# Performance work log

Measured on AMD Instinct MI355X. Metric: run time of the kernel, lower is better.

## Reference

```python
import jax, jax.numpy as jnp
import numpy as np

B, S, HID, NH, CACHE = 2, 1024, 1024, 16, 4096
HD = HID // NH
HOT = max(4, CACHE // 4)
COLD = CACHE - HOT
COMP = HID // 2
EPS = 1e-5


def setup_inputs() -> dict:
    key = jax.random.key(0)
    ks = jax.random.split(key, 16)
    std = 0.02
    inp = {
        'inputs': jax.random.normal(ks[0], (B, S, HID), jnp.float32),
        'hot_keys': std * jax.random.normal(ks[1], (HOT, HID), jnp.float32),
        'hot_values': std * jax.random.normal(ks[2], (HOT, HID), jnp.float32),
        'hot_age': jnp.zeros((HOT,), jnp.float32),
        'hot_access': jnp.zeros((HOT,), jnp.float32),
        'cold_keys': std * jax.random.normal(ks[3], (COLD, HID), jnp.float32),
        'cold_values': std * jax.random.normal(ks[4], (COLD, HID), jnp.float32),
        'cold_age': jnp.zeros((COLD,), jnp.float32),
        'cold_access': jnp.zeros((COLD,), jnp.float32),
        # linear weights stored [in, out] (y = x @ W + b)
        'Wq': std * jax.random.normal(ks[5], (HID, HID), jnp.float32),
        'bq': jnp.zeros((HID,), jnp.float32),
        'Wk': std * jax.random.normal(ks[6], (HID, HID), jnp.float32),
        'bk': jnp.zeros((HID,), jnp.float32),
        'Wv': std * jax.random.normal(ks[7], (HID, HID), jnp.float32),
        'bv': jnp.zeros((HID,), jnp.float32),
        'Wo': std * jax.random.normal(ks[8], (HID, HID), jnp.float32),
        'bo': jnp.zeros((HID,), jnp.float32),
        'Wc': (1.0 / np.sqrt(HID)) * jax.random.normal(ks[9], (HID, COMP), jnp.float32),
        'bc': jnp.zeros((COMP,), jnp.float32),
        'Wd': (1.0 / np.sqrt(COMP)) * jax.random.normal(ks[10], (COMP, HID), jnp.float32),
        'bd': jnp.zeros((HID,), jnp.float32),
        'gamma': jnp.ones((HID,), jnp.float32),
        'beta': jnp.zeros((HID,), jnp.float32),
    }
    return inp


def _cache_level(q, cache_k, v_flat, age, access, Wk, bk, Wo, bo):
    # q: [B, NH, S, HD]; cache_k/v_flat: [C, HID]
    C = cache_k.shape[0]
    k = (cache_k @ Wk + bk).reshape(C, NH, HD)
    v = v_flat.reshape(C, NH, HD)
    scores = jnp.einsum('bhsd,chd->bhsc', q, k) / np.sqrt(HD)
    scores = scores + (-0.1 * age + 0.05 * access)  # broadcast over [B,H,S,C]
    attn = jax.nn.softmax(scores, axis=-1)
    out = jnp.einsum('bhsc,chd->bhsd', attn, v)
    out = out.transpose(0, 2, 1, 3).reshape(q.shape[0], q.shape[2], HID)
    return out @ Wo + bo


def reference(inputs, hot_keys, hot_values, hot_age, hot_access,
              cold_keys, cold_values, cold_age, cold_access,
              Wq, bq, Wk, bk, Wv, bv, Wo, bo, Wc, bc, Wd, bd, gamma, beta):
    q = (inputs @ Wq + bq).reshape(B, S, NH, HD).transpose(0, 2, 1, 3)
    # hot tier: values through value_net
    hot_v = hot_values @ Wv + bv
    hot_out = _cache_level(q, hot_keys, hot_v, hot_age, hot_access, Wk, bk, Wo, bo)
    # cold tier: values through compressor -> decompressor
    cold_v = (cold_values @ Wc + bc) @ Wd + bd
    cold_out = _cache_level(q, cold_keys, cold_v, cold_age, cold_access, Wk, bk, Wo, bo)
    x = hot_out + cold_out
    mu = jnp.mean(x, axis=-1, keepdims=True)
    var = jnp.mean(jnp.square(x - mu), axis=-1, keepdims=True)
    return (x - mu) / jnp.sqrt(var + EPS) * gamma + beta
```

## Files before the change

### kernel.cpp

```cpp
#include <hip/hip_runtime.h>

#define BBATCH 2
#define SS   1024
#define HID  1024
#define NH   16
#define HD   64
#define HOT  1024
#define COLD 3072
#define COMP 512

typedef __attribute__((ext_vector_type(8))) short s8v;
typedef __attribute__((ext_vector_type(4))) float f4v;
typedef unsigned short u16;
typedef unsigned int   u32;

__device__ __forceinline__ float b2f(u16 u){ return __uint_as_float(((u32)u)<<16); }
__device__ __forceinline__ u16 f2b(float f){
  u32 u = __float_as_uint(f);
  u += 0x7FFF + ((u>>16)&1);
  return (u16)(u>>16);
}
__device__ __forceinline__ u32 pk2r(u32 a, u32 b){
  return __builtin_amdgcn_perm(b + 0x8000u, a + 0x8000u, 0x07060302u);
}
__device__ __forceinline__ float ldsc(const void* p, int i, int isf32){
  return isf32 ? ((const float*)p)[i] : b2f(((const u16*)p)[i]);
}

__global__ void detect_kernel(const u32* __restrict__ gamma_raw, u32* __restrict__ flag){
  if (threadIdx.x == 0) flag[0] = (gamma_raw[0] == 0x3F800000u) ? 1u : 0u;
}

__global__ __launch_bounds__(256) void bias_kernel(
    const void* __restrict__ h_age, const void* __restrict__ h_acc,
    const void* __restrict__ c_age, const void* __restrict__ c_acc,
    float* __restrict__ BiasH, float* __restrict__ BiasC, const u32* __restrict__ flag)
{
  const int f = (int)flag[0];
  const int i = blockIdx.x * 256 + threadIdx.x;
  if (i < HOT) BiasH[i] = -0.1f * ldsc(h_age, i, f) + 0.05f * ldsc(h_acc, i, f);
  const int j = i - HOT;
  if (j >= 0 && j < COLD) BiasC[j] = -0.1f * ldsc(c_age, j, f) + 0.05f * ldsc(c_acc, j, f);
}

struct CDesc { const void* S; u16* D; int tile0, pad; };
struct CBatch { CDesc d[5]; int nd; };

__global__ __launch_bounds__(256) void convert_multi(CBatch cb, const u32* __restrict__ flag)
{
  int di = 0;
  for (int i = 1; i < cb.nd; i++) if ((int)blockIdx.x >= cb.d[i].tile0) di = i;
  const CDesc g = cb.d[di];
  const int f = (int)flag[0];
  const size_t e0 = (size_t)(blockIdx.x - g.tile0) * 2048 + (size_t)threadIdx.x * 8;
  if (f) {
    const float* s = (const float*)g.S + e0;
    const uint4 x = *(const uint4*)s, y = *(const uint4*)(s + 4);
    *(uint4*)(g.D + e0) =
      (uint4){ pk2r(x.x,x.y), pk2r(x.z,x.w), pk2r(y.x,y.y), pk2r(y.z,y.w) };
  } else {
    *(uint4*)(g.D + e0) = *(const uint4*)((const u16*)g.S + e0);
  }
}

struct TDesc { const void* S; u16* D; int R, C, cshift, tile0; };
struct TBatch { TDesc d[6]; int nd; };

__global__ __launch_bounds__(256) void transpose_kernel(TBatch tb, const u32* __restrict__ flag)
{
  __shared__ __align__(16) u16 Tt[64][72];
  int di = 0;
  for (int i = 1; i < tb.nd; i++) if ((int)blockIdx.x >= tb.d[i].tile0) di = i;
  const TDesc g = tb.d[di];
  const int local = blockIdx.x - g.tile0;
  const int ty = local >> g.cshift;
  const int tx = local & ((1 << g.cshift) - 1);
  const int r0 = ty * 64, c0 = tx * 64;
  const int f = (int)flag[0];
  const int t = threadIdx.x;
  const int sr = t >> 2, sc = (t & 3) * 16;

  union { uint4 q[2]; u16 h[16]; } u;
  if (f) {
    const float* s = (const float*)g.S + (size_t)(r0 + sr) * g.C + c0 + sc;
    const uint4 a = *(const uint4*)s,     b = *(const uint4*)(s + 4);
    const uint4 c = *(const uint4*)(s + 8), d2 = *(const uint4*)(s + 12);
    u.q[0] = (uint4){ pk2r(a.x,a.y), pk2r(a.z,a.w), pk2r(b.x,b.y), pk2r(b.z,b.w) };
    u.q[1] = (uint4){ pk2r(c.x,c.y), pk2r(c.z,c.w), pk2r(d2.x,d2.y), pk2r(d2.z,d2.w) };
  } else {
    const u16* s = (const u16*)g.S + (size_t)(r0 + sr) * g.C + c0 + sc;
    u.q[0] = *(const uint4*)s;  u.q[1] = *(const uint4*)(s + 8);
  }
  #pragma unroll
  for (int i = 0; i < 16; i++) Tt[sc + i][sr] = u.h[i];
  __syncthreads();

  const int dc = t >> 2, dr = (t & 3) * 16;
  const uint4 o0 = *(const uint4*)&Tt[dc][dr];
  const uint4 o1 = *(const uint4*)&Tt[dc][dr + 8];
  u16* dp = g.D + (size_t)(c0 + dc) * g.R + r0 + dr;
  *(uint4*)dp = o0;  *(uint4*)(dp + 8) = o1;
}

#define BM 128
#define BN 64
#define BK 32
struct GemmDesc {
  const void* A; const u16* BT; const void* bias; u16* C;
  int aflag, bcol0, M, N, K, nxlog, tile0, ctrans;
  float bias_scale;
};
struct GemmBatch { GemmDesc d[6]; int nd; };

__global__ __launch_bounds__(256) void gemm_multi(GemmBatch bat, const u32* __restrict__ flag)
{
  __shared__ __align__(16) u16 As[BM][BK + 8];
  __shared__ __align__(16) u16 Bs[BN][BK + 8];

  int di = 0;
  for (int i = 1; i < bat.nd; i++) if ((int)blockIdx.x >= bat.d[i].tile0) di = i;
  const GemmDesc g = bat.d[di];
  const int local = blockIdx.x - g.tile0;
  const int ty = local >> g.nxlog;
  const int tx = local - (ty << g.nxlog);
  const int m0 = ty * BM, n0 = tx * BN;

  const int f  = (int)flag[0];
  const int af = g.aflag ? f : 0;

  const int tid  = threadIdx.x;
  const int lane = tid & 63, wave = tid >> 6;
  const int quad = lane >> 4, l15 = lane & 15;
  const int wy = wave >> 1, wx = wave & 1;

  f4v acc[4][2];
  #pragma unroll
  for (int i = 0; i < 4; i++)
    #pragma unroll
    for (int j = 0; j < 2; j++) acc[i][j] = (f4v){0.f,0.f,0.f,0.f};

  const int ar = tid >> 1, ac = (tid & 1) * 16;
  const int br = tid >> 2, bc = (tid & 3) * 8;

  uint4 a0, a1, a2, a3;
  uint4 b0;

  auto load_tile = [&](int kk) {
    if (af) {
      const float* s = (const float*)g.A + (size_t)(m0 + ar) * g.K + kk + ac;
      a0 = *(const uint4*)s;       a1 = *(const uint4*)(s + 4);
      a2 = *(const uint4*)(s + 8); a3 = *(const uint4*)(s + 12);
    } else {
      const u16* s = (const u16*)g.A + (size_t)(m0 + ar) * g.K + kk + ac;
      a0 = *(const uint4*)s;  a1 = *(const uint4*)(s + 8);
    }
    const u16* bs = g.BT + (size_t)(g.bcol0 + n0 + br) * g.K + kk + bc;
    b0 = *(const uint4*)bs;
  };

  load_tile(0);

  for (int k0 = 0; k0 < g.K; k0 += BK) {
    __syncthreads();
    if (af) {
      *(uint4*)&As[ar][ac] =
        (uint4){ pk2r(a0.x,a0.y), pk2r(a0.z,a0.w), pk2r(a1.x,a1.y), pk2r(a1.z,a1.w) };
      *(uint4*)&As[ar][ac + 8] =
        (uint4){ pk2r(a2.x,a2.y), pk2r(a2.z,a2.w), pk2r(a3.x,a3.y), pk2r(a3.z,a3.w) };
    } else {
      *(uint4*)&As[ar][ac] = a0;  *(uint4*)&As[ar][ac + 8] = a1;
    }
    *(uint4*)&Bs[br][bc] = b0;
    __syncthreads();

    if (k0 + BK < g.K) load_tile(k0 + BK);

    s8v afr[4], bfr[2];
    #pragma unroll
    for (int i = 0; i < 4; i++)
      afr[i] = *(const s8v*)&As[wy * 64 + i * 16 + l15][quad * 8];
    #pragma unroll
    for (int j = 0; j < 2; j++)
      bfr[j] = *(const s8v*)&Bs[wx * 32 + j * 16 + l15][quad * 8];

    #pragma unroll
    for (int j = 0; j < 2; j++)
      #pragma unroll
      for (int i = 0; i < 4; i++)
        acc[i][j] = __builtin_amdgcn_mfma_f32_16x16x32_bf16(afr[i], bfr[j], acc[i][j], 0, 0, 0);
  }

  if (g.ctrans) {
    #pragma unroll
    for (int j = 0; j < 2; j++) {
      const int col = n0 + wx * 32 + j * 16 + l15;
      const float bv = ldsc(g.bias, g.bcol0 + col, f) * g.bias_scale;
      #pragma unroll
      for (int i = 0; i < 4; i++) {
        const int row = m0 + wy * 64 + i * 16 + quad * 4;
        u16 t4[4];
        #pragma unroll
        for (int r = 0; r < 4; r++) t4[r] = f2b(acc[i][j][r] + bv);
        *(uint2*)&g.C[(size_t)col * g.M + row] = *(uint2*)t4;
      }
    }
  } else {
    #pragma unroll
    for (int j = 0; j < 2; j++) {
      const int col = n0 + wx * 32 + j * 16 + l15;
      const float bv = ldsc(g.bias, g.bcol0 + col, f) * g.bias_scale;
      #pragma unroll
      for (int i = 0; i < 4; i++) {
        const int row = m0 + wy * 64 + i * 16 + quad * 4;
        #pragma unroll
        for (int r = 0; r < 4; r++)
          g.C[(size_t)(row + r) * g.N + col] = f2b(acc[i][j][r] + bv);
      }
    }
  }
}

__global__ __launch_bounds__(256) void attn_kernel(
    const u16* __restrict__ Q,
    const u16* __restrict__ KHg, const u16* __restrict__ VHT,
    const u16* __restrict__ KCg, const u16* __restrict__ VCT,
    const float* __restrict__ BiasH, const float* __restrict__ BiasC,
    float* __restrict__ HotOut, float* __restrict__ ColdNum, float* __restrict__ ColdZ,
    int NG, int glog)
{
  __shared__ __align__(16) u16 Ks[64][72];
  __shared__ __align__(16) u16 Vs[64][72];
  __shared__ __align__(16) u16 Ps[64][72];

  const int tid  = threadIdx.x;
  const int lane = tid & 63, wave = tid >> 6;
  const int quad = lane >> 4, l15 = lane & 15;
  const int bx    = blockIdx.x;
  const int slice = bx & 3;
  const int sblk  = (bx >> 2) & 15;
  const int h     = (bx >> 6) & ((1 << glog) - 1);
  const int b     = bx >> (6 + glog);
  const int rowbase = b * SS + sblk * 64;
  const int hoff  = h * HD;
  const int myrow = wave * 16;

  const bool hot = (slice == 0);
  const u16*  Kt   = hot ? KHg : KCg;
  const u16*  Vt   = hot ? VHT : VCT;
  const float* Bias = hot ? BiasH : BiasC;
  const int   e0  = hot ? 0 : (slice - 1) * 1024;
  const int   ldv = hot ? HOT : COLD;

  const u16* qp = Q + (size_t)(rowbase + myrow + l15) * NG + hoff + quad * 8;
  const s8v aq0 = *(const s8v*)qp;
  const s8v aq1 = *(const s8v*)(qp + 32);

  const int rk = tid >> 2, sk = (tid & 3) * 16;
  const u16* kbase = Kt + (size_t)(e0 + rk) * NG + hoff + sk;
  const u16* vbase = Vt + (size_t)(hoff + rk) * ldv + e0 + sk;
  uint4 kr0 = *(const uint4*)kbase, kr1 = *(const uint4*)(kbase + 8);
  uint4 vr0 = *(const uint4*)vbase, vr1 = *(const uint4*)(vbase + 8);

  f4v o[4];
  #pragma unroll
  for (int j = 0; j < 4; j++) o[j] = (f4v){0.f,0.f,0.f,0.f};
  float z[4] = {0.f,0.f,0.f,0.f};

  for (int c0 = 0; c0 < 1024; c0 += 64) {
    __syncthreads();
    *(uint4*)&Ks[rk][sk] = kr0;  *(uint4*)&Ks[rk][sk + 8] = kr1;
    *(uint4*)&Vs[rk][sk] = vr0;  *(uint4*)&Vs[rk][sk + 8] = vr1;
    __syncthreads();
    if (c0 + 64 < 1024) {
      const u16* kn = kbase + (size_t)(c0 + 64) * NG;
      const u16* vn = vbase + (c0 + 64);
      kr0 = *(const uint4*)kn;  kr1 = *(const uint4*)(kn + 8);
      vr0 = *(const uint4*)vn;  vr1 = *(const uint4*)(vn + 8);
    }

    #pragma unroll
    for (int j = 0; j < 4; j++) {
      f4v s = (f4v){0.f,0.f,0.f,0.f};
      const s8v bk0 = *(const s8v*)&Ks[j * 16 + l15][quad * 8];
      const s8v bk1 = *(const s8v*)&Ks[j * 16 + l15][32 + quad * 8];
      s = __builtin_amdgcn_mfma_f32_16x16x32_bf16(aq0, bk0, s, 0, 0, 0);
      s = __builtin_amdgcn_mfma_f32_16x16x32_bf16(aq1, bk1, s, 0, 0, 0);
      const int cg = e0 + c0 + j * 16 + l15;
      const float bias = Bias[cg];
      #pragma unroll
      for (int r = 0; r < 4; r++) {
        const float ev = __expf(fminf(s[r] * 0.125f + bias, 30.f));
        z[r] += ev;
        Ps[myrow + quad * 4 + r][j * 16 + l15] =
            (u16)((__float_as_uint(ev) + 0x8000u) >> 16);
      }
    }
    const s8v ap0 = *(const s8v*)&Ps[myrow + l15][quad * 8];
    const s8v ap1 = *(const s8v*)&Ps[myrow + l15][32 + quad * 8];
    #pragma unroll
    for (int j = 0; j < 4; j++) {
      const s8v bv0 = *(const s8v*)&Vs[j * 16 + l15][quad * 8];
      const s8v bv1 = *(const s8v*)&Vs[j * 16 + l15][32 + quad * 8];
      o[j] = __builtin_amdgcn_mfma_f32_16x16x32_bf16(ap0, bv0, o[j], 0, 0, 0);
      o[j] = __builtin_amdgcn_mfma_f32_16x16x32_bf16(ap1, bv1, o[j], 0, 0, 0);
    }
  }

  #pragma unroll
  for (int m = 1; m < 16; m <<= 1)
    #pragma unroll
    for (int r = 0; r < 4; r++) z[r] += __shfl_xor(z[r], m, 64);

  if (hot) {
    float rz[4];
    #pragma unroll
    for (int r = 0; r < 4; r++) rz[r] = 1.0f / z[r];
    #pragma unroll
    for (int j = 0; j < 4; j++) {
      const int col = hoff + j * 16 + l15;
      #pragma unroll
      for (int r = 0; r < 4; r++) {
        const int row = rowbase + myrow + quad * 4 + r;
        HotOut[(size_t)row * NG + col] = o[j][r] * rz[r];
      }
    }
  } else {
    #pragma unroll
    for (int j = 0; j < 4; j++) {
      const int col = hoff + j * 16 + l15;
      #pragma unroll
      for (int r = 0; r < 4; r++) {
        const int row = rowbase + myrow + quad * 4 + r;
        atomicAdd(&ColdNum[(size_t)row * NG + col], o[j][r]);
      }
    }
    if (l15 == 0) {
      #pragma unroll
      for (int r = 0; r < 4; r++) {
        const int row = rowbase + myrow + quad * 4 + r;
        atomicAdd(&ColdZ[(size_t)row * (1 << glog) + h], z[r]);
      }
    }
  }
}

__global__ __launch_bounds__(256) void combine_kernel(
    const float* __restrict__ HotOut, float* __restrict__ ColdNum,
    float* __restrict__ ColdZ, u16* __restrict__ ATT,
    int att_ld, int att_c0, int NG, int glog)
{
  const int gid   = blockIdx.x * 256 + threadIdx.x;
  const int shift = 4 + glog;
  const int row   = gid >> shift;
  const int c4    = (gid & ((1 << shift) - 1)) << 2;
  const int h     = c4 >> 6;
  const int G     = 1 << glog;

  const float4 hv = *(const float4*)&HotOut[(size_t)row * NG + c4];
  float4* cp = (float4*)&ColdNum[(size_t)row * NG + c4];
  const float4 cn = *cp;
  const float zi = 1.0f / ColdZ[(size_t)row * G + h];

  u16 ov[4];
  ov[0] = f2b(hv.x + cn.x * zi); ov[1] = f2b(hv.y + cn.y * zi);
  ov[2] = f2b(hv.z + cn.z * zi); ov[3] = f2b(hv.w + cn.w * zi);
  *(uint2*)&ATT[(size_t)row * att_ld + att_c0 + c4] = *(uint2*)ov;

  *cp = (float4){0.f,0.f,0.f,0.f};
  if ((c4 & 63) == 0) ColdZ[(size_t)row * G + h] = 0.f;
}

__global__ __launch_bounds__(256) void ln_kernel(
    const u16* __restrict__ X, const void* __restrict__ gamma,
    const void* __restrict__ beta, void* __restrict__ outp,
    const u32* __restrict__ flag)
{
  __shared__ float red[4];
  const int f = (int)flag[0];
  const int row = blockIdx.x, tid = threadIdx.x;
  const u16* xr = X + (size_t)row * HID;

  float x[4];
  { union { uint2 q; u16 hx[4]; } bx2;
    bx2.q = *(const uint2*)(xr + tid * 4);
    #pragma unroll
    for (int i = 0; i < 4; i++) x[i] = b2f(bx2.hx[i]); }

  float s = x[0] + x[1] + x[2] + x[3];
  #pragma unroll
  for (int m = 1; m < 64; m <<= 1) s += __shfl_xor(s, m, 64);
  if ((tid & 63) == 0) red[tid >> 6] = s;
  __syncthreads();
  const float mu = (red[0] + red[1] + red[2] + red[3]) * (1.0f / HID);
  __syncthreads();

  float v = 0.f;
  #pragma unroll
  for (int i = 0; i < 4; i++) { const float d = x[i] - mu; v += d * d; }
  #pragma unroll
  for (int m = 1; m < 64; m <<= 1) v += __shfl_xor(v, m, 64);
  if ((tid & 63) == 0) red[tid >> 6] = v;
  __syncthreads();
  const float var  = (red[0] + red[1] + red[2] + red[3]) * (1.0f / HID);
  const float rstd = 1.0f / sqrtf(var + 1e-5f);

  #pragma unroll
  for (int i = 0; i < 4; i++) {
    const int col = tid * 4 + i;
    const float val = (x[i] - mu) * rstd * ldsc(gamma, col, f) + ldsc(beta, col, f);
    if (f) ((float*)outp)[(size_t)row * HID + col] = val;
    else   ((u16*) outp)[(size_t)row * HID + col] = f2b(val);
  }
}

extern "C" void kernel_launch(void* const* d_in, const int* in_sizes, int n_in,
                              void* d_out, int out_size, void* d_ws, size_t ws_size,
                              hipStream_t stream)
{
  const void* inputs      = d_in[0];
  const void* hot_keys    = d_in[1];
  const void* hot_values  = d_in[2];
  const void* hot_age     = d_in[3];
  const void* hot_access  = d_in[4];
  const void* cold_keys   = d_in[5];
  const void* cold_values = d_in[6];
  const void* cold_age    = d_in[7];
  const void* cold_access = d_in[8];
  const void* Wq = d_in[9];   const void* bq = d_in[10];
  const void* Wk = d_in[11];  const void* bk = d_in[12];
  const void* Wv = d_in[13];  const void* bv = d_in[14];
  const void* Wo = d_in[15];  const void* bo = d_in[16];
  const void* Wc = d_in[17];  const void* bc = d_in[18];
  const void* Wd = d_in[19];  const void* bd = d_in[20];
  const void* gamma = d_in[21];
  const void* beta  = d_in[22];

  const size_t FIX    = 256 + 16384;
  const size_t WT     = (size_t)10 * 1024 * 1024;
  const size_t COPIES = (size_t)10240 * 1024 * 2;
  const size_t XB     = (size_t)2048 * HID * 2;
  auto PART = [](int Gc){ return (size_t)2048 * (64 * Gc) * 8 + (size_t)2048 * Gc * 4; };
  auto BUFS = [](int Gc){ return (size_t)10240 * (64 * Gc) * 2; };
  auto MX   = [](size_t a, size_t b){ return a > b ? a : b; };

  int G = 0, docopy = 0;
  { const size_t needF = FIX + WT + MX(COPIES, MX(PART(16), XB)) + BUFS(16);
    if (ws_size >= needF) { G = 16; docopy = 1; } }
  for (int c = 8; c >= 2 && !G; c >>= 1)
    if (ws_size >= FIX + WT + COPIES + MX(PART(c), XB) + BUFS(c)) { G = c; docopy = 1; }
  for (int c = 8; c >= 2 && !G; c >>= 1)
    if (ws_size >= FIX + WT + MX(PART(c), XB) + BUFS(c)) { G = c; docopy = 0; }
  if (!G) return;
  const int glog = (G == 16) ? 4 : (G == 8 ? 3 : (G == 4 ? 2 : 1));
  const int NG = 64 * G;
  const bool full = (G == 16);

  char* base  = (char*)d_ws;
  u32*  flag  = (u32*)base;
  float* BiasH = (float*)(base + 256);
  float* BiasC = BiasH + HOT;
  u16* WqT = (u16*)(base + FIX);
  u16* WkT = WqT + (size_t)1024 * 1024;
  u16* WvT = WkT + (size_t)1024 * 1024;
  u16* WoT = WvT + (size_t)1024 * 1024;
  u16* WcT = WoT + (size_t)1024 * 1024;
  u16* WdT = WcT + (size_t)512 * 1024;
  char* rp0 = base + FIX + WT;

  u16* inputsB = (u16*)rp0;
  u16* hotkB   = inputsB + (size_t)2048 * 1024;
  u16* coldkB  = hotkB   + (size_t)1024 * 1024;
  u16* hotvB   = coldkB  + (size_t)3072 * 1024;
  u16* coldvB  = hotvB   + (size_t)1024 * 1024;

  char* rp = rp0 + ((docopy && !full) ? COPIES : 0);
  u16*   X       = (u16*)rp;
  float* HotOut  = (float*)rp;
  float* ColdNum = (float*)(rp + (size_t)2048 * NG * 4);
  float* ColdZ   = (float*)(rp + (size_t)2048 * NG * 8);
  const size_t Rbytes = full ? MX(COPIES, MX(PART(16), XB)) : MX(PART(G), XB);
  u16* Qg  = (u16*)(rp + Rbytes);
  u16* KHg = Qg  + (size_t)2048 * NG;
  u16* KCg = KHg + (size_t)HOT  * NG;
  u16* VHT = KCg + (size_t)COLD * NG;
  u16* VCT = VHT + (size_t)HOT  * NG;
  u16* ATT   = (u16*)d_out;
  u16* CVmid = (u16*)d_out + (size_t)2048 * 1024;

  const void* Aq = docopy ? (const void*)inputsB : inputs;
  const void* Ahk = docopy ? (const void*)hotkB  : hot_keys;
  const void* Ack = docopy ? (const void*)coldkB : cold_keys;
  const void* Ahv = docopy ? (const void*)hotvB  : hot_values;
  const void* Acv = docopy ? (const void*)coldvB : cold_values;
  const int afl = docopy ? 0 : 1;

  const dim3 blk(256);
  const int mQ = 2048 / BM, mH = HOT / BM, mC = COLD / BM;
  const size_t coldPart = (size_t)2048 * NG * 4 + (size_t)2048 * G * 4;

  detect_kernel<<<dim3(1), dim3(64), 0, stream>>>((const u32*)gamma, flag);
  bias_kernel<<<dim3((HOT + COLD) / 256), blk, 0, stream>>>(
      hot_age, hot_access, cold_age, cold_access, BiasH, BiasC, flag);

  if (docopy) {
    CBatch cb; cb.nd = 5; int t = 0;
    cb.d[0] = { inputs,      inputsB, t, 0 }; t += 1024;
    cb.d[1] = { hot_keys,    hotkB,   t, 0 }; t += 512;
    cb.d[2] = { cold_keys,   coldkB,  t, 0 }; t += 1536;
    cb.d[3] = { hot_values,  hotvB,   t, 0 }; t += 512;
    cb.d[4] = { cold_values, coldvB,  t, 0 }; t += 1536;
    convert_multi<<<dim3(t), blk, 0, stream>>>(cb, flag);
  }
  { TBatch tb; tb.nd = 6; int t = 0;
    tb.d[0] = { Wq, WqT, 1024, 1024, 4, t }; t += 256;
    tb.d[1] = { Wk, WkT, 1024, 1024, 4, t }; t += 256;
    tb.d[2] = { Wv, WvT, 1024, 1024, 4, t }; t += 256;
    tb.d[3] = { Wo, WoT, 1024, 1024, 4, t }; t += 256;
    tb.d[4] = { Wc, WcT, 1024,  512, 3, t }; t += 128;
    tb.d[5] = { Wd, WdT,  512, 1024, 4, t }; t += 128;
    transpose_kernel<<<dim3(t), blk, 0, stream>>>(tb, flag);
  }

  if (full) {
    { GemmBatch bb; bb.nd = 5; int t = 0;
      bb.d[0] = { Aq,  WqT, bq, Qg,    afl, 0, 2048, 1024, 1024, 4, t, 0, 1.0f }; t += 16 * mQ;
      bb.d[1] = { Ahk, WkT, bk, KHg,   afl, 0, HOT,  1024, 1024, 4, t, 0, 1.0f }; t += 16 * mH;
      bb.d[2] = { Ack, WkT, bk, KCg,   afl, 0, COLD, 1024, 1024, 4, t, 0, 1.0f }; t += 16 * mC;
      bb.d[3] = { Ahv, WvT, bv, VHT,   afl, 0, HOT,  1024, 1024, 4, t, 1, 1.0f }; t += 16 * mH;
      bb.d[4] = { Acv, WcT, bc, CVmid, afl, 0, COLD,  512, 1024, 3, t, 0, 1.0f }; t += 8 * mC;
      gemm_multi<<<dim3(t), blk, 0, stream>>>(bb, flag);
    }
    { GemmBatch bb; bb.nd = 1;
      bb.d[0] = { CVmid, WdT, bd, VCT, 0, 0, COLD, 1024, 512, 4, 0, 1, 1.0f };
      gemm_multi<<<dim3(16 * mC), blk, 0, stream>>>(bb, flag);
    }
    hipMemsetAsync(ColdNum, 0, coldPart, stream);
    attn_kernel<<<dim3(BBATCH * 16 * 16 * 4), blk, 0, stream>>>(
        Qg, KHg, VHT, KCg, VCT, BiasH, BiasC, HotOut, ColdNum, ColdZ, NG, glog);
    combine_kernel<<<dim3((2048 * (NG / 4)) / 256), blk, 0, stream>>>(
        HotOut, ColdNum, ColdZ, ATT, HID, 0, NG, glog);
  } else {
    hipMemsetAsync(ColdNum, 0, coldPart, stream);
    { GemmBatch bb; bb.nd = 5; int t = 0;
      bb.d[0] = { Aq,  WqT, bq, Qg,    afl, 0, 2048, NG,  1024, glog, t, 0, 1.0f }; t += G * mQ;
      bb.d[1] = { Ahk, WkT, bk, KHg,   afl, 0, HOT,  NG,  1024, glog, t, 0, 1.0f }; t += G * mH;
      bb.d[2] = { Ack, WkT, bk, KCg,   afl, 0, COLD, NG,  1024, glog, t, 0, 1.0f }; t += G * mC;
      bb.d[3] = { Ahv, WvT, bv, VHT,   afl, 0, HOT,  NG,  1024, glog, t, 1, 1.0f }; t += G * mH;
      bb.d[4] = { Acv, WcT, bc, CVmid, afl, 0, COLD, 512, 1024, 3,    t, 0, 1.0f }; t += 8 * mC;
      gemm_multi<<<dim3(t), blk, 0, stream>>>(bb, flag);
    }
    { GemmBatch bb; bb.nd = 1;
      bb.d[0] = { CVmid, WdT, bd, VCT, 0, 0, COLD, NG, 512, glog, 0, 1, 1.0f };
      gemm_multi<<<dim3(G * mC), blk, 0, stream>>>(bb, flag);
    }
    attn_kernel<<<dim3(BBATCH * G * 16 * 4), blk, 0, stream>>>(
        Qg, KHg, VHT, KCg, VCT, BiasH, BiasC, HotOut, ColdNum, ColdZ, NG, glog);
    combine_kernel<<<dim3((2048 * (NG / 4)) / 256), blk, 0, stream>>>(
        HotOut, ColdNum, ColdZ, ATT, HID, 0, NG, glog);

    for (int p = 1; p < NH / G; ++p) {
      const int c0 = p * NG;
      GemmBatch bb; bb.nd = 5; int t = 0;
      bb.d[0] = { Aq,    WqT, bq, Qg,  afl, c0, 2048, NG, 1024, glog, t, 0, 1.0f }; t += G * mQ;
      bb.d[1] = { Ahk,   WkT, bk, KHg, afl, c0, HOT,  NG, 1024, glog, t, 0, 1.0f }; t += G * mH;
      bb.d[2] = { Ack,   WkT, bk, KCg, afl, c0, COLD, NG, 1024, glog, t, 0, 1.0f }; t += G * mC;
      bb.d[3] = { Ahv,   WvT, bv, VHT, afl, c0, HOT,  NG, 1024, glog, t, 1, 1.0f }; t += G * mH;
      bb.d[4] = { CVmid, WdT, bd, VCT, 0,   c0, COLD, NG, 512,  glog, t, 1, 1.0f }; t += G * mC;
      gemm_multi<<<dim3(t), blk, 0, stream>>>(bb, flag);

      attn_kernel<<<dim3(BBATCH * G * 16 * 4), blk, 0, stream>>>(
          Qg, KHg, VHT, KCg, VCT, BiasH, BiasC, HotOut, ColdNum, ColdZ, NG, glog);
      combine_kernel<<<dim3((2048 * (NG / 4)) / 256), blk, 0, stream>>>(
          HotOut, ColdNum, ColdZ, ATT, HID, c0, NG, glog);
    }
  }

  { GemmBatch bb; bb.nd = 1;
    bb.d[0] = { ATT, WoT, bo, X, 0, 0, 2048, 1024, 1024, 4, 0, 0, 2.0f };
    gemm_multi<<<dim3(16 * mQ), blk, 0, stream>>>(bb, flag);
  }
  ln_kernel<<<dim3(2048), blk, 0, stream>>>(X, gamma, beta, d_out, flag);
}
```

Before: 320.0 us.

## Keep attention probabilities in registers via transposed QK MFMA and lane shuffles

Computes S^T = K·Q^T so each lane holds scores for one query row across keys, then packs exp values to bf16 and redistributes them with cross-lane shuffles into the MFMA A-operand layout for the P·V product. This removes the Ps shared-memory buffer and its write/read round trip, reduces the row-sum to a per-lane scalar, and vectorizes bias loads. It also sets launch bounds to request 8 waves-per-EU occupancy, which may increase register pressure or spilling.

```diff
diff --git a/kernel.cpp b/kernel.cpp
--- a/kernel.cpp
+++ b/kernel.cpp
@@ -220,7 +220,7 @@
   }
 }
 
-__global__ __launch_bounds__(256) void attn_kernel(
+__global__ __launch_bounds__(256, 8) void attn_kernel(
     const u16* __restrict__ Q,
     const u16* __restrict__ KHg, const u16* __restrict__ VHT,
     const u16* __restrict__ KCg, const u16* __restrict__ VCT,
@@ -230,7 +230,6 @@
 {
   __shared__ __align__(16) u16 Ks[64][72];
   __shared__ __align__(16) u16 Vs[64][72];
-  __shared__ __align__(16) u16 Ps[64][72];
 
   const int tid  = threadIdx.x;
   const int lane = tid & 63, wave = tid >> 6;
@@ -264,7 +263,7 @@
   f4v o[4];
   #pragma unroll
   for (int j = 0; j < 4; j++) o[j] = (f4v){0.f,0.f,0.f,0.f};
-  float z[4] = {0.f,0.f,0.f,0.f};
+  float zs = 0.f;
 
   for (int c0 = 0; c0 < 1024; c0 += 64) {
     __syncthreads();
@@ -279,42 +278,60 @@
     }
 
     #pragma unroll
-    for (int j = 0; j < 4; j++) {
-      f4v s = (f4v){0.f,0.f,0.f,0.f};
-      const s8v bk0 = *(const s8v*)&Ks[j * 16 + l15][quad * 8];
-      const s8v bk1 = *(const s8v*)&Ks[j * 16 + l15][32 + quad * 8];
-      s = __builtin_amdgcn_mfma_f32_16x16x32_bf16(aq0, bk0, s, 0, 0, 0);
-      s = __builtin_amdgcn_mfma_f32_16x16x32_bf16(aq1, bk1, s, 0, 0, 0);
-      const int cg = e0 + c0 + j * 16 + l15;
-      const float bias = Bias[cg];
-      #pragma unroll
-      for (int r = 0; r < 4; r++) {
-        const float ev = __expf(fminf(s[r] * 0.125f + bias, 30.f));
-        z[r] += ev;
-        Ps[myrow + quad * 4 + r][j * 16 + l15] =
-            (u16)((__float_as_uint(ev) + 0x8000u) >> 16);
+    for (int h2 = 0; h2 < 2; h2++) {
+      const s8v ka0 = *(const s8v*)&Ks[h2 * 32 + l15][quad * 8];
+      const s8v ka1 = *(const s8v*)&Ks[h2 * 32 + l15][32 + quad * 8];
+      const s8v kb0 = *(const s8v*)&Ks[h2 * 32 + 16 + l15][quad * 8];
+      const s8v kb1 = *(const s8v*)&Ks[h2 * 32 + 16 + l15][32 + quad * 8];
+      f4v s0 = (f4v){0.f,0.f,0.f,0.f}, s1 = (f4v){0.f,0.f,0.f,0.f};
+      s0 = __builtin_amdgcn_mfma_f32_16x16x32_bf16(ka0, aq0, s0, 0, 0, 0);
+      s0 = __builtin_amdgcn_mfma_f32_16x16x32_bf16(ka1, aq1, s0, 0, 0, 0);
+      s1 = __builtin_amdgcn_mfma_f32_16x16x32_bf16(kb0, aq0, s1, 0, 0, 0);
+      s1 = __builtin_amdgcn_mfma_f32_16x16x32_bf16(kb1, aq1, s1, 0, 0, 0);
+
+      const int cg0 = e0 + c0 + h2 * 32 + quad * 4;
+      const float4 bi0 = *(const float4*)&Bias[cg0];
+      const float4 bi1 = *(const float4*)&Bias[cg0 + 16];
+      float p0[4], p1[4];
+      p0[0] = __expf(fminf(s0[0] * 0.125f + bi0.x, 30.f));
+      p0[1] = __expf(fminf(s0[1] * 0.125f + bi0.y, 30.f));
+      p0[2] = __expf(fminf(s0[2] * 0.125f + bi0.z, 30.f));
+      p0[3] = __expf(fminf(s0[3] * 0.125f + bi0.w, 30.f));
+      p1[0] = __expf(fminf(s1[0] * 0.125f + bi1.x, 30.f));
+      p1[1] = __expf(fminf(s1[1] * 0.125f + bi1.y, 30.f));
+      p1[2] = __expf(fminf(s1[2] * 0.125f + bi1.z, 30.f));
+      p1[3] = __expf(fminf(s1[3] * 0.125f + bi1.w, 30.f));
+      zs += p0[0] + p0[1] + p0[2] + p0[3] + p1[0] + p1[1] + p1[2] + p1[3];
+
+      const u32 W0 = pk2r(__float_as_uint(p0[0]), __float_as_uint(p0[1]));
+      const u32 W1 = pk2r(__float_as_uint(p0[2]), __float_as_uint(p0[3]));
+      const u32 W2 = pk2r(__float_as_uint(p1[0]), __float_as_uint(p1[1]));
+      const u32 W3 = pk2r(__float_as_uint(p1[2]), __float_as_uint(p1[3]));
+
+      union { u32 w[4]; s8v v; } ap;
+      #pragma unroll
+      for (int t = 0; t < 4; t++) {
+        const int srcl = (((quad << 1) + (t >> 1)) & 3) * 16 + l15;
+        const u32 lo = __shfl((t & 1) ? W1 : W0, srcl, 64);
+        const u32 hi = __shfl((t & 1) ? W3 : W2, srcl, 64);
+        ap.w[t] = (quad >= 2) ? hi : lo;
       }
-    }
-    const s8v ap0 = *(const s8v*)&Ps[myrow + l15][quad * 8];
-    const s8v ap1 = *(const s8v*)&Ps[myrow + l15][32 + quad * 8];
-    #pragma unroll
-    for (int j = 0; j < 4; j++) {
-      const s8v bv0 = *(const s8v*)&Vs[j * 16 + l15][quad * 8];
-      const s8v bv1 = *(const s8v*)&Vs[j * 16 + l15][32 + quad * 8];
-      o[j] = __builtin_amdgcn_mfma_f32_16x16x32_bf16(ap0, bv0, o[j], 0, 0, 0);
-      o[j] = __builtin_amdgcn_mfma_f32_16x16x32_bf16(ap1, bv1, o[j], 0, 0, 0);
-    }
-  }
-
-  #pragma unroll
-  for (int m = 1; m < 16; m <<= 1)
-    #pragma unroll
-    for (int r = 0; r < 4; r++) z[r] += __shfl_xor(z[r], m, 64);
+
+      #pragma unroll
+      for (int j2 = 0; j2 < 4; j2++) {
+        const s8v bv = *(const s8v*)&Vs[j2 * 16 + l15][h2 * 32 + quad * 8];
+        o[j2] = __builtin_amdgcn_mfma_f32_16x16x32_bf16(ap.v, bv, o[j2], 0, 0, 0);
+      }
+    }
+  }
+
+  zs += __shfl_xor(zs, 16, 64);
+  zs += __shfl_xor(zs, 32, 64);
 
   if (hot) {
     float rz[4];
     #pragma unroll
-    for (int r = 0; r < 4; r++) rz[r] = 1.0f / z[r];
+    for (int r = 0; r < 4; r++) rz[r] = 1.0f / __shfl(zs, quad * 4 + r, 64);
     #pragma unroll
     for (int j = 0; j < 4; j++) {
       const int col = hoff + j * 16 + l15;
@@ -334,13 +351,8 @@
         atomicAdd(&ColdNum[(size_t)row * NG + col], o[j][r]);
       }
     }
-    if (l15 == 0) {
-      #pragma unroll
-      for (int r = 0; r < 4; r++) {
-        const int row = rowbase + myrow + quad * 4 + r;
-        atomicAdd(&ColdZ[(size_t)row * (1 << glog) + h], z[r]);
-      }
-    }
+    if (lane < 16)
+      atomicAdd(&ColdZ[(size_t)(rowbase + myrow + lane) * (1 << glog) + h], zs);
   }
 }
 
```

Result: slower. 468.8 us (+46.5%).
